# Kernel tuning notes

Measured on AMD Instinct MI355X. Metric: run time of the kernel, lower is better.

The kernel has to match this reference:

```python
import jax, jax.numpy as jnp
import numpy as np

N, MAX_SIZE, SPATIAL = 50000, 32, 27
CH_IN, CH_OUT = 128, 128


def setup_inputs() -> dict:
    key = jax.random.key(0)
    k1, k2, k3, k4 = jax.random.split(key, 4)
    feat_in = jax.random.normal(k1, (N, CH_IN), dtype=jnp.float32)
    select_mat = jax.random.uniform(k2, (N, MAX_SIZE, SPATIAL), dtype=jnp.float32)
    # kaiming-uniform-ish init for weight of shape [SPATIAL, CH_OUT*CH_IN]
    fan_in = CH_OUT * CH_IN
    bound = np.sqrt(6.0 / fan_in)
    weight = jax.random.uniform(k3, (SPATIAL, CH_OUT * CH_IN), dtype=jnp.float32,
                                minval=-bound, maxval=bound)
    neighbor_idx = jax.random.randint(k4, (N, MAX_SIZE), 0, N, dtype=jnp.int64)
    return {"feat_in": feat_in, "select_mat": select_mat,
            "weight": weight, "neighbor_idx": neighbor_idx}


def reference(feat_in, select_mat, weight, neighbor_idx):
    # feat_in: [N, I]; select_mat: [N, M, S]; weight: [S, O*I]; neighbor_idx: [N, M]
    ch_in = feat_in.shape[1]
    spatial = weight.shape[0]
    ch_out = weight.shape[1] // ch_in
    w = weight.reshape(spatial, ch_out, ch_in)          # [S, O, I]
    patch_feat = feat_in[neighbor_idx]                  # irregular gather -> [N, M, I]
    # Original math: out[n,o] = sum_m sum_s sel[n,m,s] * W[s,o,i] * pf[n,m,i]
    # Contract neighbor dim first to avoid the [N, M, O, I] intermediate.
    t = jnp.einsum('nms,nmi->nsi', select_mat, patch_feat)   # [N, S, I]
    feat_out = jnp.einsum('nsi,soi->no', t, w)               # [N, O]
    return feat_out[:, :, None]                              # [N, O, 1]
```

## Files before the change

kernel.cpp:

```cpp
#include <hip/hip_runtime.h>


#define N_CHI 128
#define N_SP  27
#define N_M   32
#define KDIM  (N_SP * N_CHI)
#define SEL_STRIDE (N_M * N_SP)

typedef short s16x8 __attribute__((ext_vector_type(8)));
typedef s16x8 __attribute__((may_alias)) s16x8_a;
typedef unsigned short u16x8 __attribute__((ext_vector_type(8)));
typedef u16x8 __attribute__((may_alias)) u16x8_a;
typedef unsigned int u32x2 __attribute__((ext_vector_type(2)));
typedef u32x2 __attribute__((may_alias)) u32x2_a;
typedef float f32x4 __attribute__((ext_vector_type(4)));
typedef f32x4 __attribute__((may_alias)) f32x4_a;
typedef float f32x16 __attribute__((ext_vector_type(16)));

typedef __attribute__((address_space(3))) unsigned int as3_u32;
typedef __attribute__((address_space(1))) const unsigned int as1_u32;

static __device__ __forceinline__ unsigned short f2bf(float f) {
  unsigned int u = __float_as_uint(f);
  u += 0x7FFFu + ((u >> 16) & 1u);
  return (unsigned short)(u >> 16);
}

__global__ __launch_bounds__(128) void wconv_kernel(const float* __restrict__ w,
                                                    unsigned short* __restrict__ Wt) {
  const int s = blockIdx.x;
  const int o = blockIdx.y;
  const int i = threadIdx.x;
  Wt[((size_t)o * N_SP + s) * N_CHI + i] = f2bf(w[((size_t)s * 128 + o) * N_CHI + i]);
}

__global__ __launch_bounds__(256) void featbf_kernel(const float* __restrict__ feat,
                                                     unsigned short* __restrict__ fb,
                                                     int total4) {
  const int i = blockIdx.x * 256 + threadIdx.x;
  if (i >= total4) return;
  f32x4 v = *(const f32x4_a*)&feat[(size_t)i * 4];
  u32x2 o;
  o[0] = (unsigned int)f2bf(v[0]) | ((unsigned int)f2bf(v[1]) << 16);
  o[1] = (unsigned int)f2bf(v[2]) | ((unsigned int)f2bf(v[3]) << 16);
  *(u32x2_a*)&fb[(size_t)i * 4] = o;
}

__global__ __launch_bounds__(256, 5) void phase1_kernel(
    const unsigned short* __restrict__ featbf, const float* __restrict__ sel,
    const int* __restrict__ nidx, unsigned short* __restrict__ T,
    int nbase, int nend) {
  __shared__ __align__(16) unsigned short tbuf[4][N_SP * 128];
  const int wave = threadIdx.x >> 6;
  const int lane = threadIdx.x & 63;
  const int n = nbase + (int)blockIdx.x * 4 + wave;
  if (n >= nend) return;
  unsigned short* tb = tbuf[wave];
  const int q = lane >> 5;
  const int col = lane & 31;
  const bool sv = (col < N_SP);

  const float* selp = sel + (size_t)n * SEL_STRIDE;
  s16x8 bf0, bf1;
#pragma unroll
  for (int j = 0; j < 8; ++j) {
    const int m0 = q * 8 + j;
    float v0 = sv ? selp[m0 * N_SP + col] : 0.0f;
    float v1 = sv ? selp[(16 + m0) * N_SP + col] : 0.0f;
    bf0[j] = (short)f2bf(v0);
    bf1[j] = (short)f2bf(v1);
  }

  const int* ip = nidx + (size_t)n * N_M;
  int offe[16];
#pragma unroll
  for (int ks = 0; ks < 2; ++ks)
#pragma unroll
    for (int j = 0; j < 8; ++j)
      offe[ks * 8 + j] = ip[ks * 16 + q * 8 + j] * N_CHI;

#pragma unroll
  for (int ti = 0; ti < 4; ++ti) {
    const int icol = ti * 32 + col;
    s16x8 af0, af1;
#pragma unroll
    for (int j = 0; j < 8; ++j) {
      af0[j] = (short)featbf[offe[j] + icol];
      af1[j] = (short)featbf[offe[8 + j] + icol];
    }
    f32x16 acc = {0.f, 0.f, 0.f, 0.f, 0.f, 0.f, 0.f, 0.f,
                  0.f, 0.f, 0.f, 0.f, 0.f, 0.f, 0.f, 0.f};
    acc = __builtin_amdgcn_mfma_f32_32x32x16_bf16(af0, bf0, acc, 0, 0, 0);
    acc = __builtin_amdgcn_mfma_f32_32x32x16_bf16(af1, bf1, acc, 0, 0, 0);
    if (sv) {
#pragma unroll
      for (int g = 0; g < 4; ++g) {
        const int sub = ti * 8 + g * 2 + q;
        const int phys = col * 128 + (((sub ^ ((col & 7) << 2))) << 2);
        u32x2 pk;
        pk[0] = (unsigned int)f2bf(acc[4 * g + 0]) | ((unsigned int)f2bf(acc[4 * g + 1]) << 16);
        pk[1] = (unsigned int)f2bf(acc[4 * g + 2]) | ((unsigned int)f2bf(acc[4 * g + 3]) << 16);
        *(u32x2_a*)&tb[phys] = pk;
      }
    }
  }

  unsigned short* Tn = T + (size_t)(n - nbase) * KDIM;
#pragma unroll
  for (int it = 0; it < 7; ++it) {
    const int P = it * 64 + lane;
    if (P < 432) {
      const int c = P >> 4;
      const int sub = (P << 1) & 31;
      const int phys = c * 128 + (((sub ^ ((c & 7) << 2))) << 2);
      *(u16x8_a*)&Tn[(size_t)P * 8] = *(const u16x8_a*)&tb[phys];
    }
  }
}

__global__ __launch_bounds__(256, 4) void phase2_kernel(
    const unsigned short* __restrict__ T, const unsigned short* __restrict__ Wt,
    float* __restrict__ out, int nbase, int N) {
  __shared__ __align__(16) unsigned short Alds[64 * 64];
  __shared__ __align__(16) unsigned short Blds[128 * 64];
  const int tid = threadIdx.x;
  const int lane = tid & 63;
  const int wbase = tid & ~63;
  const int wave = tid >> 6;
  const int wm = wave & 1, wn = wave >> 1;
  const int quad = lane >> 4, l16 = lane & 15;
  const size_t rowbase = (size_t)blockIdx.x * 64;

  f32x4 acc[2][4];
#pragma unroll
  for (int a = 0; a < 2; ++a)
#pragma unroll
    for (int b = 0; b < 4; ++b) acc[a][b] = (f32x4){0.f, 0.f, 0.f, 0.f};

  const unsigned short* aga[2];
  const unsigned short* bga[4];
#pragma unroll
  for (int it = 0; it < 2; ++it) {
    const int slot = it * 256 + tid;
    const int r = slot >> 3, bp = slot & 7;
    aga[it] = T + (rowbase + r) * KDIM + ((bp ^ (r & 7)) << 3);
  }
#pragma unroll
  for (int it = 0; it < 4; ++it) {
    const int slot = it * 256 + tid;
    const int r = slot >> 3, bp = slot & 7;
    bga[it] = Wt + (size_t)r * KDIM + ((bp ^ (r & 7)) << 3);
  }

  const int NKT = KDIM / 64;
  for (int kt = 0; kt < NKT; ++kt) {
    const int k0 = kt * 64;
#pragma unroll
    for (int it = 0; it < 2; ++it)
      __builtin_amdgcn_global_load_lds(
          (as1_u32*)(const void*)(aga[it] + k0),
          (as3_u32*)(void*)&Alds[(it * 256 + wbase) * 8], 16, 0, 0);
#pragma unroll
    for (int it = 0; it < 4; ++it)
      __builtin_amdgcn_global_load_lds(
          (as1_u32*)(const void*)(bga[it] + k0),
          (as3_u32*)(void*)&Blds[(it * 256 + wbase) * 8], 16, 0, 0);
    __syncthreads();
#pragma unroll
    for (int ks = 0; ks < 2; ++ks) {
      const int bg = ks * 4 + quad;
      s16x8 af[2], bfr[4];
#pragma unroll
      for (int mt = 0; mt < 2; ++mt) {
        const int m = wm * 32 + mt * 16 + l16;
        af[mt] = *(const s16x8_a*)&Alds[m * 64 + ((bg ^ (m & 7)) << 3)];
      }
#pragma unroll
      for (int nt = 0; nt < 4; ++nt) {
        const int o = wn * 64 + nt * 16 + l16;
        bfr[nt] = *(const s16x8_a*)&Blds[o * 64 + ((bg ^ (o & 7)) << 3)];
      }
#pragma unroll
      for (int mt = 0; mt < 2; ++mt)
#pragma unroll
        for (int nt = 0; nt < 4; ++nt)
          acc[mt][nt] = __builtin_amdgcn_mfma_f32_16x16x32_bf16(af[mt], bfr[nt],
                                                                acc[mt][nt], 0, 0, 0);
    }
    __syncthreads();
  }

#pragma unroll
  for (int mt = 0; mt < 2; ++mt) {
    const int growb = nbase + (int)rowbase + wm * 32 + mt * 16 + quad * 4;
#pragma unroll
    for (int r = 0; r < 4; ++r) {
      const int grow = growb + r;
      if (grow < N) {
#pragma unroll
        for (int nt = 0; nt < 4; ++nt) {
          const int o = wn * 64 + nt * 16 + l16;
          out[(size_t)grow * 128 + o] = acc[mt][nt][r];
        }
      }
    }
  }
}

extern "C" void kernel_launch(void* const* d_in, const int* in_sizes, int n_in,
                              void* d_out, int out_size, void* d_ws, size_t ws_size,
                              hipStream_t stream) {
  const float* feat = (const float*)d_in[0];
  const float* sel  = (const float*)d_in[1];
  const float* wgt  = (const float*)d_in[2];
  const int*   nidx = (const int*)d_in[3];
  float* out = (float*)d_out;
  const int N = in_sizes[0] / N_CHI;

  unsigned short* Wt = (unsigned short*)d_ws;
  const size_t WT_ELEMS = (size_t)128 * KDIM;
  unsigned short* FB = Wt + WT_ELEMS;
  const size_t FB_ELEMS = (size_t)N * N_CHI;
  unsigned short* T = FB + FB_ELEMS;

  wconv_kernel<<<dim3(N_SP, 128), 128, 0, stream>>>(wgt, Wt);
  const int total4 = (int)(FB_ELEMS / 4);
  featbf_kernel<<<dim3((unsigned)((total4 + 255) / 256)), 256, 0, stream>>>(
      feat, FB, total4);

  const size_t used = (WT_ELEMS + FB_ELEMS) * 2;
  const size_t bytes_for_T = (ws_size > used) ? (ws_size - used) : 0;
  long cap_rows = (long)(bytes_for_T / ((size_t)KDIM * 2));
  long NC = (cap_rows / 128) * 128;
  const long Nfull = (((long)N + 127) / 128) * 128;
  if (NC > Nfull) NC = Nfull;
  if (NC <= 0) return;

  for (long nb = 0; nb < N; nb += NC) {
    long rows = (long)N - nb;
    if (rows > NC) rows = NC;
    const long rows64 = ((rows + 63) / 64) * 64;
    phase1_kernel<<<dim3((unsigned)((rows + 3) / 4)), 256, 0, stream>>>(
        FB, sel, nidx, T, (int)nb, (int)(nb + rows));
    phase2_kernel<<<dim3((unsigned)(rows64 / 64)), 256, 0, stream>>>(
        T, Wt, out, (int)nb, N);
  }
}
```

Before: 498.3 us.

## Triple-buffer phase2 LDS loads, fuse prep kernels, cap chunk size

The phase2 GEMM now keeps three LDS stages. It prefetches two k-tiles ahead with global_load_lds and uses manual vmcnt waits plus one barrier per iteration, so loads overlap MFMA compute instead of being serialized behind two syncs. The weight and feature bf16 conversion kernels are merged into a single launch. The chunk size is capped at 25088 rows, so T is processed in two chunks and may stay more cache-resident. The extra buffers raise LDS use per block to 72KB and reduce occupancy, and the launch-bounds occupancy hint is dropped.

```diff
diff --git a/kernel.cpp b/kernel.cpp
--- a/kernel.cpp
+++ b/kernel.cpp
@@ -26,24 +26,26 @@
   return (unsigned short)(u >> 16);
 }
 
-__global__ __launch_bounds__(128) void wconv_kernel(const float* __restrict__ w,
-                                                    unsigned short* __restrict__ Wt) {
-  const int s = blockIdx.x;
-  const int o = blockIdx.y;
-  const int i = threadIdx.x;
-  Wt[((size_t)o * N_SP + s) * N_CHI + i] = f2bf(w[((size_t)s * 128 + o) * N_CHI + i]);
-}
-
-__global__ __launch_bounds__(256) void featbf_kernel(const float* __restrict__ feat,
-                                                     unsigned short* __restrict__ fb,
-                                                     int total4) {
-  const int i = blockIdx.x * 256 + threadIdx.x;
-  if (i >= total4) return;
-  f32x4 v = *(const f32x4_a*)&feat[(size_t)i * 4];
-  u32x2 o;
-  o[0] = (unsigned int)f2bf(v[0]) | ((unsigned int)f2bf(v[1]) << 16);
-  o[1] = (unsigned int)f2bf(v[2]) | ((unsigned int)f2bf(v[3]) << 16);
-  *(u32x2_a*)&fb[(size_t)i * 4] = o;
+__global__ __launch_bounds__(256) void prep_kernel(
+    const float* __restrict__ feat, unsigned short* __restrict__ fb, int total4,
+    const float* __restrict__ w, unsigned short* __restrict__ Wt, int fb_blks) {
+  const int b = (int)blockIdx.x;
+  if (b < fb_blks) {
+    const int i = b * 256 + (int)threadIdx.x;
+    if (i >= total4) return;
+    f32x4 v = *(const f32x4_a*)&feat[(size_t)i * 4];
+    u32x2 o;
+    o[0] = (unsigned int)f2bf(v[0]) | ((unsigned int)f2bf(v[1]) << 16);
+    o[1] = (unsigned int)f2bf(v[2]) | ((unsigned int)f2bf(v[3]) << 16);
+    *(u32x2_a*)&fb[(size_t)i * 4] = o;
+  } else {
+    const int e = (b - fb_blks) * 256 + (int)threadIdx.x;
+    const int i = e & 127;
+    const int so = e >> 7;
+    const int o = so & 127;
+    const int s = so >> 7;
+    Wt[((size_t)o * N_SP + s) * N_CHI + i] = f2bf(w[e]);
+  }
 }
 
 __global__ __launch_bounds__(256, 5) void phase1_kernel(
@@ -118,11 +120,11 @@
   }
 }
 
-__global__ __launch_bounds__(256, 4) void phase2_kernel(
+__global__ __launch_bounds__(256) void phase2_kernel(
     const unsigned short* __restrict__ T, const unsigned short* __restrict__ Wt,
     float* __restrict__ out, int nbase, int N) {
-  __shared__ __align__(16) unsigned short Alds[64 * 64];
-  __shared__ __align__(16) unsigned short Blds[128 * 64];
+  __shared__ __align__(16) unsigned short Alds[3][64 * 64];
+  __shared__ __align__(16) unsigned short Blds[3][128 * 64];
   const int tid = threadIdx.x;
   const int lane = tid & 63;
   const int wbase = tid & ~63;
@@ -152,20 +154,20 @@
     bga[it] = Wt + (size_t)r * KDIM + ((bp ^ (r & 7)) << 3);
   }
 
-  const int NKT = KDIM / 64;
-  for (int kt = 0; kt < NKT; ++kt) {
-    const int k0 = kt * 64;
+  auto stage = [&](int buf, int k0) {
 #pragma unroll
     for (int it = 0; it < 2; ++it)
       __builtin_amdgcn_global_load_lds(
           (as1_u32*)(const void*)(aga[it] + k0),
-          (as3_u32*)(void*)&Alds[(it * 256 + wbase) * 8], 16, 0, 0);
+          (as3_u32*)(void*)&Alds[buf][(it * 256 + wbase) * 8], 16, 0, 0);
 #pragma unroll
     for (int it = 0; it < 4; ++it)
       __builtin_amdgcn_global_load_lds(
           (as1_u32*)(const void*)(bga[it] + k0),
-          (as3_u32*)(void*)&Blds[(it * 256 + wbase) * 8], 16, 0, 0);
-    __syncthreads();
+          (as3_u32*)(void*)&Blds[buf][(it * 256 + wbase) * 8], 16, 0, 0);
+  };
+
+  auto compute = [&](int cur) {
 #pragma unroll
     for (int ks = 0; ks < 2; ++ks) {
       const int bg = ks * 4 + quad;
@@ -173,12 +175,12 @@
 #pragma unroll
       for (int mt = 0; mt < 2; ++mt) {
         const int m = wm * 32 + mt * 16 + l16;
-        af[mt] = *(const s16x8_a*)&Alds[m * 64 + ((bg ^ (m & 7)) << 3)];
+        af[mt] = *(const s16x8_a*)&Alds[cur][m * 64 + ((bg ^ (m & 7)) << 3)];
       }
 #pragma unroll
       for (int nt = 0; nt < 4; ++nt) {
         const int o = wn * 64 + nt * 16 + l16;
-        bfr[nt] = *(const s16x8_a*)&Blds[o * 64 + ((bg ^ (o & 7)) << 3)];
+        bfr[nt] = *(const s16x8_a*)&Blds[cur][o * 64 + ((bg ^ (o & 7)) << 3)];
       }
 #pragma unroll
       for (int mt = 0; mt < 2; ++mt)
@@ -187,7 +189,20 @@
           acc[mt][nt] = __builtin_amdgcn_mfma_f32_16x16x32_bf16(af[mt], bfr[nt],
                                                                 acc[mt][nt], 0, 0, 0);
     }
-    __syncthreads();
+  };
+
+  const int NKT = KDIM / 64;
+  stage(0, 0);
+  stage(1, 64);
+
+  for (int kt = 0; kt < NKT; ++kt) {
+    if (kt < NKT - 1) asm volatile("s_waitcnt vmcnt(6)" ::: "memory");
+    else              asm volatile("s_waitcnt vmcnt(0)" ::: "memory");
+    asm volatile("s_waitcnt lgkmcnt(0)" ::: "memory");
+    __builtin_amdgcn_s_barrier();
+    asm volatile("" ::: "memory");
+    if (kt + 2 < NKT) stage((kt + 2) % 3, (kt + 2) * 64);
+    compute(kt % 3);
   }
 
 #pragma unroll
@@ -223,15 +238,17 @@
   const size_t FB_ELEMS = (size_t)N * N_CHI;
   unsigned short* T = FB + FB_ELEMS;
 
-  wconv_kernel<<<dim3(N_SP, 128), 128, 0, stream>>>(wgt, Wt);
   const int total4 = (int)(FB_ELEMS / 4);
-  featbf_kernel<<<dim3((unsigned)((total4 + 255) / 256)), 256, 0, stream>>>(
-      feat, FB, total4);
+  const int fb_blks = (total4 + 255) / 256;
+  const int wt_blks = (N_SP * 128 * 128) / 256;
+  prep_kernel<<<dim3((unsigned)(fb_blks + wt_blks)), 256, 0, stream>>>(
+      feat, FB, total4, wgt, Wt, fb_blks);
 
   const size_t used = (WT_ELEMS + FB_ELEMS) * 2;
   const size_t bytes_for_T = (ws_size > used) ? (ws_size - used) : 0;
   long cap_rows = (long)(bytes_for_T / ((size_t)KDIM * 2));
   long NC = (cap_rows / 128) * 128;
+  if (NC > 25088) NC = 25088;
   const long Nfull = (((long)N + 127) / 128) * 128;
   if (NC > Nfull) NC = Nfull;
   if (NC <= 0) return;
```

New measurement: 512.1 us. 1.03x slower.
